# Performance work log

Measured on AMD Instinct MI355X. Metric: run time of the kernel, lower is better.

Reference implementation:

```python
import jax, jax.numpy as jnp
import numpy as np

NUM_USERS = 100000
NUM_ITEMS = 50000
N_NODES = NUM_USERS + NUM_ITEMS
N_EDGES = 2_000_000
D = 64          # embedding_dim
HEADS = 4
F1 = D // HEADS  # per-head out dim of gat1
BATCH = 16384
NEG_SLOPE = 0.2  # PyG GATConv default negative_slope


def setup_inputs() -> dict:
    key = jax.random.key(0)
    ks = jax.random.split(key, 13)
    inp = {}
    inp["edge_index"] = jax.random.randint(ks[0], (2, N_EDGES), 0, N_NODES, dtype=jnp.int64)
    inp["batch_user_idx"] = jax.random.randint(ks[1], (BATCH,), 0, NUM_USERS, dtype=jnp.int64)
    inp["batch_item_idx"] = jax.random.randint(ks[2], (BATCH,), 0, NUM_ITEMS, dtype=jnp.int64)
    # Embedding tables (nn.init.normal_ std=0.01)
    inp["user_emb"] = 0.01 * jax.random.normal(ks[3], (NUM_USERS, D), dtype=jnp.float32)
    inp["item_emb"] = 0.01 * jax.random.normal(ks[4], (NUM_ITEMS, D), dtype=jnp.float32)
    # gat1: GATConv(64, 16, heads=4, concat=True)
    inp["W1"] = jax.random.normal(ks[5], (D, HEADS * F1), dtype=jnp.float32) / np.sqrt(D)
    inp["a_src1"] = jax.random.normal(ks[6], (HEADS, F1), dtype=jnp.float32) / np.sqrt(F1)
    inp["a_dst1"] = jax.random.normal(ks[7], (HEADS, F1), dtype=jnp.float32) / np.sqrt(F1)
    inp["b1"] = jnp.zeros((HEADS * F1,), dtype=jnp.float32)
    # gat2: GATConv(64, 64, heads=1)
    inp["W2"] = jax.random.normal(ks[8], (D, D), dtype=jnp.float32) / np.sqrt(D)
    inp["a_src2"] = jax.random.normal(ks[9], (1, D), dtype=jnp.float32) / np.sqrt(D)
    inp["a_dst2"] = jax.random.normal(ks[10], (1, D), dtype=jnp.float32) / np.sqrt(D)
    inp["b2"] = jnp.zeros((D,), dtype=jnp.float32)
    return inp


def _gat_conv(x, src, dst, W, a_src, a_dst, b, num_nodes):
    """PyG GATConv (eval mode, concat, self-loops already in src/dst)."""
    H, F = a_src.shape
    h = (x @ W).reshape(num_nodes, H, F)                 # [N,H,F]
    alpha_s = jnp.einsum('nhf,hf->nh', h, a_src)         # [N,H]
    alpha_d = jnp.einsum('nhf,hf->nh', h, a_dst)
    e = alpha_s[src] + alpha_d[dst]                      # [E,H]
    e = jax.nn.leaky_relu(e, NEG_SLOPE)
    # scatter-softmax over destination neighborhoods
    m = jax.ops.segment_max(e, dst, num_segments=num_nodes)   # [N,H]
    e = jnp.exp(e - m[dst])
    denom = jax.ops.segment_sum(e, dst, num_segments=num_nodes)
    alpha = e / denom[dst]                               # [E,H]
    msg = h[src] * alpha[:, :, None]                     # [E,H,F]
    agg = jax.ops.segment_sum(msg, dst, num_segments=num_nodes)  # [N,H,F]
    return agg.reshape(num_nodes, H * F) + b


def reference(user_emb, item_emb, W1, a_src1, a_dst1, b1,
              W2, a_src2, a_dst2, b2,
              edge_index, batch_user_idx, batch_item_idx):
    x = jnp.concatenate([user_emb, item_emb], axis=0)    # [N,D]
    n = x.shape[0]
    loop = jnp.arange(n, dtype=edge_index.dtype)          # add_self_loops=True
    src = jnp.concatenate([edge_index[0], loop])
    dst = jnp.concatenate([edge_index[1], loop])
    x = jax.nn.elu(_gat_conv(x, src, dst, W1, a_src1, a_dst1, b1, n))
    x = jax.nn.elu(_gat_conv(x, src, dst, W2, a_src2, a_dst2, b2, n))
    u = x[batch_user_idx]
    v = x[batch_item_idx + NUM_USERS]
    return jax.nn.sigmoid(jnp.sum(u * v, axis=1))        # [BATCH]
```

## Files before the change

kernel.cpp:

```cpp
#include <hip/hip_runtime.h>
#include <math.h>

#define SHIFT 8
#define NBMAX 1024
#define CAP   4096
#define TILE  8192
#define HSCALE 64.0f

typedef float v2f __attribute__((ext_vector_type(2)));
typedef short bf16x8 __attribute__((ext_vector_type(8)));
typedef float f32x4 __attribute__((ext_vector_type(4)));

__device__ __forceinline__ unsigned short f2bf(float f) {
    unsigned u = __float_as_uint(f);
    unsigned r = u + 0x7FFFu + ((u >> 16) & 1u);
    return (unsigned short)(r >> 16);
}
__device__ __forceinline__ unsigned pack2bf(float lo, float hi) {
    return (unsigned)f2bf(lo) | ((unsigned)f2bf(hi) << 16);
}
__device__ __forceinline__ float bflo(unsigned u) { return __uint_as_float(u << 16); }
__device__ __forceinline__ float bfhi(unsigned u) { return __uint_as_float(u & 0xFFFF0000u); }


__global__ __launch_bounds__(512) void k_partition(
    const int* __restrict__ src, const int* __restrict__ dst, int E,
    unsigned* __restrict__ gcur, unsigned* __restrict__ pairs, int NB,
    const float* __restrict__ W1, const float* __restrict__ W2,
    unsigned short* __restrict__ WT1, unsigned short* __restrict__ WT2) {
    __shared__ unsigned lh[NBMAX];
    __shared__ unsigned lcur[NBMAX];
    int t = threadIdx.x;
    {
        int gt = blockIdx.x * 512 + t;
        if (gt < 4096) {
            int n = gt & 63, k = gt >> 6;
            WT1[n * 64 + k] = f2bf(W1[k * 64 + n]);
            WT2[n * 64 + k] = f2bf(W2[k * 64 + n]);
        }
    }
    for (int q = t; q < NB; q += 512) lh[q] = 0;
    __syncthreads();
    int base = blockIdx.x * TILE;
    int end = min(E, base + TILE);
    for (int i = base + t; i < end; i += 512)
        atomicAdd(&lh[((unsigned)dst[i]) >> SHIFT], 1u);
    __syncthreads();
    for (int q = t; q < NB; q += 512) {
        unsigned c = lh[q];
        lcur[q] = c ? ((unsigned)q * CAP + atomicAdd(&gcur[q], c)) : 0u;
    }
    __syncthreads();
    for (int i = base + t; i < end; i += 512) {
        unsigned d = (unsigned)dst[i];
        unsigned pos = atomicAdd(&lcur[d >> SHIFT], 1u);
        pairs[pos] = ((d & 255u) << 18) | (unsigned)src[i];
    }
}

__global__ __launch_bounds__(512) void k_buck_lin(
    const unsigned* __restrict__ pairs, const unsigned* __restrict__ gcur,
    unsigned* __restrict__ beg, unsigned* __restrict__ endd,
    int* __restrict__ srt, int N, int NB,
    const float* __restrict__ xa, const float* __restrict__ xb, int split,
    const unsigned short* __restrict__ WTg,
    const float* __restrict__ a_src, const float* __restrict__ a_dst,
    unsigned char* __restrict__ h, float* __restrict__ as_out,
    float* __restrict__ ad_out) {
    __shared__ union U {
        struct { unsigned lh[256]; unsigned lcur[256]; unsigned sh[256]; int ssrt[CAP]; } b;
        struct { unsigned short sX[64 * 72]; unsigned short sWT[64 * 72]; float sH[64 * 68]; } l;
    } u;
    int t = threadIdx.x;

    if ((int)blockIdx.x < NB) {
        int b = blockIdx.x;
        unsigned s0 = (unsigned)b * CAP;
        int cnt = (int)gcur[b];
        if (t < 256) u.b.lh[t] = 0;
        __syncthreads();
        for (int i = t; i < cnt; i += 512)
            atomicAdd(&u.b.lh[pairs[s0 + i] >> 18], 1u);
        __syncthreads();
        unsigned deg_t = 0;
        if (t < 256) { deg_t = u.b.lh[t]; u.b.sh[t] = deg_t; }
        __syncthreads();
        for (int off = 1; off < 256; off <<= 1) {
            unsigned x = 0;
            if (t < 256 && t >= off) x = u.b.sh[t - off];
            __syncthreads();
            if (t < 256) u.b.sh[t] += x;
            __syncthreads();
        }
        if (t < 256) {
            unsigned excl = u.b.sh[t] - deg_t;
            u.b.lcur[t] = excl;
            int node = (b << SHIFT) + t;
            if (node < N) { beg[node] = s0 + excl; endd[node] = s0 + excl + deg_t; }
        }
        __syncthreads();
        for (int i = t; i < cnt; i += 512) {
            unsigned pk = pairs[s0 + i];
            unsigned p = atomicAdd(&u.b.lcur[pk >> 18], 1u);
            u.b.ssrt[p] = (int)(pk & 0x3FFFFu);
        }
        __syncthreads();
        for (int i = t; i < cnt; i += 512) srt[s0 + i] = u.b.ssrt[i];
    } else {
        int nodeBase = ((int)blockIdx.x - NB) * 64;
        {
            int r = t >> 3, c8 = (t & 7) * 8;
            int n = nodeBase + r;
            float4 v0 = {0,0,0,0}, v1 = {0,0,0,0};
            if (n < N) {
                const float* row = (n < split) ? (xa + (size_t)n * 64 + c8)
                                               : (xb + (size_t)(n - split) * 64 + c8);
                const float4* r4 = (const float4*)row;
                v0 = r4[0]; v1 = r4[1];
            }
            uint4 A = make_uint4(pack2bf(v0.x, v0.y), pack2bf(v0.z, v0.w),
                                 pack2bf(v1.x, v1.y), pack2bf(v1.z, v1.w));
            *(uint4*)(void*)(u.l.sX + r * 72 + c8) = A;
            const uint4* wsrc = (const uint4*)(const void*)WTg;
            *(uint4*)(void*)(u.l.sWT + r * 72 + c8) = wsrc[r * 8 + (c8 >> 3)];
        }
        __syncthreads();
        {
            int lane = t & 63, w = t >> 6;
            if (w < 4) {
                int gl = lane & 15, quad = lane >> 4;
                int m0 = w * 16;
                const bf16x8 a0 = *(const bf16x8*)(void*)(u.l.sX + (m0 + gl) * 72 + quad * 8);
                const bf16x8 a1 = *(const bf16x8*)(void*)(u.l.sX + (m0 + gl) * 72 + 32 + quad * 8);
                f32x4 acc[4];
#pragma unroll
                for (int tt = 0; tt < 4; ++tt) {
                    const bf16x8 b0 = *(const bf16x8*)(void*)(u.l.sWT + (tt * 16 + gl) * 72 + quad * 8);
                    const bf16x8 b1 = *(const bf16x8*)(void*)(u.l.sWT + (tt * 16 + gl) * 72 + 32 + quad * 8);
                    f32x4 c = {0.f, 0.f, 0.f, 0.f};
                    c = __builtin_amdgcn_mfma_f32_16x16x32_bf16(a0, b0, c, 0, 0, 0);
                    c = __builtin_amdgcn_mfma_f32_16x16x32_bf16(a1, b1, c, 0, 0, 0);
                    acc[tt] = c;
                }
#pragma unroll
                for (int tt = 0; tt < 4; ++tt)
#pragma unroll
                    for (int rr = 0; rr < 4; ++rr)
                        u.l.sH[(m0 + quad * 4 + rr) * 68 + tt * 16 + gl] = acc[tt][rr];
            }
        }
        __syncthreads();
        if (t < 256) {
            int m = t >> 2, p = t & 3;
            int n = nodeBase + m;
            const float4* sp = (const float4*)(void*)(u.l.sH + m * 68 + p * 16);
            float4 q0 = sp[0], q1 = sp[1], q2 = sp[2], q3 = sp[3];
            float hv[16] = {q0.x,q0.y,q0.z,q0.w, q1.x,q1.y,q1.z,q1.w,
                            q2.x,q2.y,q2.z,q2.w, q3.x,q3.y,q3.z,q3.w};
            if (n < N) {
                unsigned dwords[4];
#pragma unroll
                for (int q = 0; q < 4; ++q) {
                    int d0 = __builtin_amdgcn_cvt_pk_fp8_f32(hv[4*q] * HSCALE, hv[4*q+1] * HSCALE, 0, false);
                    d0 = __builtin_amdgcn_cvt_pk_fp8_f32(hv[4*q+2] * HSCALE, hv[4*q+3] * HSCALE, d0, true);
                    dwords[q] = (unsigned)d0;
                }
                ((uint4*)h)[(size_t)n * 4 + p] = make_uint4(dwords[0], dwords[1], dwords[2], dwords[3]);
                float ps = 0.f, pd = 0.f;
#pragma unroll
                for (int i = 0; i < 16; ++i) {
                    ps = fmaf(hv[i], a_src[p * 16 + i], ps);
                    pd = fmaf(hv[i], a_dst[p * 16 + i], pd);
                }
                as_out[n * 4 + p] = ps;
                ad_out[n * 4 + p] = pd;
            }
        }
    }
}


template <int HT, int BIN>
__global__ __launch_bounds__(256) void k_linear_mfma(
    const void* __restrict__ xav, const void* __restrict__ xbv, int split,
    const unsigned short* __restrict__ WTg,
    const float* __restrict__ a_src, const float* __restrict__ a_dst,
    unsigned char* __restrict__ h, float* __restrict__ as_out,
    float* __restrict__ ad_out, int N) {
    __shared__ unsigned short sX[64 * 72];
    __shared__ unsigned short sWT[64 * 72];
    __shared__ float sH[64 * 68];
    int t = threadIdx.x;
    int nodeBase = blockIdx.x * 64;

    {
        int r = t >> 2, c4 = (t & 3) * 16;
        int n = nodeBase + r;
        uint4 A = {0,0,0,0}, Bv = {0,0,0,0};
        if (BIN) {
            if (n < N) {
                const unsigned short* row = (const unsigned short*)xav + (size_t)n * 64 + c4;
                A  = ((const uint4*)(const void*)row)[0];
                Bv = ((const uint4*)(const void*)row)[1];
            }
        } else {
            float4 v0 = {0,0,0,0}, v1 = {0,0,0,0}, v2 = {0,0,0,0}, v3 = {0,0,0,0};
            if (n < N) {
                const float* row = (n < split) ? ((const float*)xav + (size_t)n * 64 + c4)
                                               : ((const float*)xbv + (size_t)(n - split) * 64 + c4);
                const float4* r4 = (const float4*)row;
                v0 = r4[0]; v1 = r4[1]; v2 = r4[2]; v3 = r4[3];
            }
            A  = make_uint4(pack2bf(v0.x, v0.y), pack2bf(v0.z, v0.w),
                            pack2bf(v1.x, v1.y), pack2bf(v1.z, v1.w));
            Bv = make_uint4(pack2bf(v2.x, v2.y), pack2bf(v2.z, v2.w),
                            pack2bf(v3.x, v3.y), pack2bf(v3.z, v3.w));
        }
        *(uint4*)(void*)(sX + r * 72 + c4) = A;
        *(uint4*)(void*)(sX + r * 72 + c4 + 8) = Bv;
        const uint4* wsrc = (const uint4*)(const void*)WTg;
        int base = (r * 64 + c4) >> 3;
        *(uint4*)(void*)(sWT + r * 72 + c4) = wsrc[base];
        *(uint4*)(void*)(sWT + r * 72 + c4 + 8) = wsrc[base + 1];
    }
    __syncthreads();

    {
        int lane = t & 63, w = t >> 6;
        int gl = lane & 15, quad = lane >> 4;
        int m0 = w * 16;
        const bf16x8 a0 = *(const bf16x8*)(void*)(sX + (m0 + gl) * 72 + quad * 8);
        const bf16x8 a1 = *(const bf16x8*)(void*)(sX + (m0 + gl) * 72 + 32 + quad * 8);
        f32x4 acc[4];
#pragma unroll
        for (int tt = 0; tt < 4; ++tt) {
            const bf16x8 b0 = *(const bf16x8*)(void*)(sWT + (tt * 16 + gl) * 72 + quad * 8);
            const bf16x8 b1 = *(const bf16x8*)(void*)(sWT + (tt * 16 + gl) * 72 + 32 + quad * 8);
            f32x4 c = {0.f, 0.f, 0.f, 0.f};
            c = __builtin_amdgcn_mfma_f32_16x16x32_bf16(a0, b0, c, 0, 0, 0);
            c = __builtin_amdgcn_mfma_f32_16x16x32_bf16(a1, b1, c, 0, 0, 0);
            acc[tt] = c;
        }
#pragma unroll
        for (int tt = 0; tt < 4; ++tt)
#pragma unroll
            for (int rr = 0; rr < 4; ++rr)
                sH[(m0 + quad * 4 + rr) * 68 + tt * 16 + gl] = acc[tt][rr];
    }
    __syncthreads();

    {
        int m = t >> 2, p = t & 3;
        int n = nodeBase + m;
        const float4* sp = (const float4*)(void*)(sH + m * 68 + p * 16);
        float4 q0 = sp[0], q1 = sp[1], q2 = sp[2], q3 = sp[3];
        float hv[16] = {q0.x,q0.y,q0.z,q0.w, q1.x,q1.y,q1.z,q1.w,
                        q2.x,q2.y,q2.z,q2.w, q3.x,q3.y,q3.z,q3.w};
        if (n < N) {
            unsigned dwords[4];
#pragma unroll
            for (int q = 0; q < 4; ++q) {
                int d0 = __builtin_amdgcn_cvt_pk_fp8_f32(hv[4*q] * HSCALE, hv[4*q+1] * HSCALE, 0, false);
                d0 = __builtin_amdgcn_cvt_pk_fp8_f32(hv[4*q+2] * HSCALE, hv[4*q+3] * HSCALE, d0, true);
                dwords[q] = (unsigned)d0;
            }
            ((uint4*)h)[(size_t)n * 4 + p] = make_uint4(dwords[0], dwords[1], dwords[2], dwords[3]);
            float ps = 0.f, pd = 0.f;
#pragma unroll
            for (int i = 0; i < 16; ++i) {
                ps = fmaf(hv[i], a_src[p * 16 + i], ps);
                pd = fmaf(hv[i], a_dst[p * 16 + i], pd);
            }
            if (HT == 4) {
                as_out[n * 4 + p] = ps;
                ad_out[n * 4 + p] = pd;
            } else {
                ps += __shfl_xor(ps, 1, 64); ps += __shfl_xor(ps, 2, 64);
                pd += __shfl_xor(pd, 1, 64); pd += __shfl_xor(pd, 2, 64);
                if (p == 0) { as_out[n] = ps; ad_out[n] = pd; }
            }
        }
    }
}

template <int HT>
__global__ __launch_bounds__(256, 4) void k_gat(
                      const int* __restrict__ srt, const unsigned* __restrict__ beg,
                      const unsigned* __restrict__ endd,
                      const unsigned* __restrict__ hq, const float* __restrict__ as,
                      const float* __restrict__ ad, const float* __restrict__ b,
                      unsigned* __restrict__ xout, int N) {
    __shared__ unsigned s_vo[4][4][40];
    __shared__ float    s_w[4][4][(HT == 4) ? 164 : 40];

    int t = threadIdx.x;
    int lane = t & 63;
    int wv = t >> 6;
    int gl = lane & 15;
    int g  = lane >> 4;
    int wid = (int)((blockIdx.x * blockDim.x + t) >> 6);
    int d = wid * 4 + g;
    bool active = d < N;
    const int hh = (HT == 4) ? (gl >> 2) : 0;
    const unsigned gl4 = (unsigned)gl << 2;
    const char* hqb = (const char*)hq;
    const char* asb = (const char*)as;

    float adv = 0.f, l = 0.f;
    float a0 = 0.f, a1 = 0.f, a2 = 0.f, a3 = 0.f;
    int kb = 0, end = 0;
    if (active) {
        adv = ad[d * HT + hh];
        float e0 = as[d * HT + hh] + adv;
        e0 = (e0 > 0.f) ? e0 : 0.2f * e0;
        float w0 = __expf(e0);
        unsigned dw = hq[(size_t)d * 16 + gl];
        v2f lo = __builtin_amdgcn_cvt_pk_f32_fp8((int)dw, false);
        v2f hi = __builtin_amdgcn_cvt_pk_f32_fp8((int)dw, true);
        l = w0;
        a0 = w0 * lo.x; a1 = w0 * lo.y; a2 = w0 * hi.x; a3 = w0 * hi.y;
        kb = (int)beg[d];
        end = (int)endd[d];
    }

    int m = end - kb;
    while (__ballot(m > 0)) {
        unsigned v0 = 0, v1 = 0;
        if (gl < m)      v0 = ((unsigned)srt[kb + gl]) << 6;
        if (gl + 16 < m) v1 = ((unsigned)srt[kb + gl + 16]) << 6;

        if (HT == 1) {
            float as0 = 0.f, as1 = 0.f;
            if (gl < m)      as0 = *(const float*)(asb + (v0 >> 4));
            if (gl + 16 < m) as1 = *(const float*)(asb + (v1 >> 4));
            s_vo[wv][g][gl]      = v0;
            s_vo[wv][g][gl + 16] = v1;
            asm volatile("s_waitcnt lgkmcnt(0)" ::: "memory");
            __builtin_amdgcn_sched_barrier(0);
            unsigned rr[32];
            const uint4* vob = (const uint4*)(const void*)&s_vo[wv][g][0];
#pragma unroll
            for (int c = 0; c < 8; ++c) {
                uint4 vv = vob[c];
                rr[4*c+0] = *(const unsigned*)(hqb + (vv.x + gl4));
                rr[4*c+1] = *(const unsigned*)(hqb + (vv.y + gl4));
                rr[4*c+2] = *(const unsigned*)(hqb + (vv.z + gl4));
                rr[4*c+3] = *(const unsigned*)(hqb + (vv.w + gl4));
            }
            float w0 = 0.f, w1 = 0.f;
            if (gl < m) {
                float e = as0 + adv;
                e = (e > 0.f) ? e : 0.2f * e;
                w0 = __expf(e);
            }
            if (gl + 16 < m) {
                float e = as1 + adv;
                e = (e > 0.f) ? e : 0.2f * e;
                w1 = __expf(e);
            }
            float wsum = w0 + w1;
            wsum += __shfl_xor(wsum, 1, 64);
            wsum += __shfl_xor(wsum, 2, 64);
            wsum += __shfl_xor(wsum, 4, 64);
            wsum += __shfl_xor(wsum, 8, 64);
            l += wsum;
            s_w[wv][g][gl]      = w0;
            s_w[wv][g][gl + 16] = w1;
            asm volatile("s_waitcnt lgkmcnt(0)" ::: "memory");
            __builtin_amdgcn_sched_barrier(0);
            const float4* wrd = (const float4*)(const void*)&s_w[wv][g][0];
#pragma unroll
            for (int c = 0; c < 8; ++c) {
                float4 wc = wrd[c];
                float wj[4] = {wc.x, wc.y, wc.z, wc.w};
#pragma unroll
                for (int j = 0; j < 4; ++j) {
                    float w = wj[j];
                    unsigned rv = rr[4*c + j];
                    v2f lo = __builtin_amdgcn_cvt_pk_f32_fp8((int)rv, false);
                    v2f hi = __builtin_amdgcn_cvt_pk_f32_fp8((int)rv, true);
                    a0 = fmaf(w, lo.x, a0);
                    a1 = fmaf(w, lo.y, a1);
                    a2 = fmaf(w, hi.x, a2);
                    a3 = fmaf(w, hi.y, a3);
                }
            }
        } else {
            s_vo[wv][g][gl]      = v0;
            s_vo[wv][g][gl + 16] = v1;
            asm volatile("s_waitcnt lgkmcnt(0)" ::: "memory");
            __builtin_amdgcn_sched_barrier(0);
            int eb = (gl & 3) << 3;
            const uint4* vop = (const uint4*)(const void*)&s_vo[wv][g][eb];
            uint4 va = vop[0], vb = vop[1];
            unsigned vs[8] = {va.x, va.y, va.z, va.w, vb.x, vb.y, vb.z, vb.w};
            float av[8];
#pragma unroll
            for (int r = 0; r < 8; ++r)
                av[r] = *(const float*)(asb + ((vs[r] >> 2) + ((unsigned)hh << 2)));
            unsigned rr[32];
            const uint4* vob = (const uint4*)(const void*)&s_vo[wv][g][0];
#pragma unroll
            for (int c = 0; c < 8; ++c) {
                uint4 vv = vob[c];
                rr[4*c+0] = *(const unsigned*)(hqb + (vv.x + gl4));
                rr[4*c+1] = *(const unsigned*)(hqb + (vv.y + gl4));
                rr[4*c+2] = *(const unsigned*)(hqb + (vv.z + gl4));
                rr[4*c+3] = *(const unsigned*)(hqb + (vv.w + gl4));
            }
            float wq[8];
#pragma unroll
            for (int r = 0; r < 8; ++r) {
                wq[r] = 0.f;
                if (eb + r < m) {
                    float e = av[r] + adv;
                    e = (e > 0.f) ? e : 0.2f * e;
                    wq[r] = __expf(e);
                }
            }
            float wsum = ((wq[0] + wq[1]) + (wq[2] + wq[3]))
                       + ((wq[4] + wq[5]) + (wq[6] + wq[7]));
            wsum += __shfl_xor(wsum, 1, 64);
            wsum += __shfl_xor(wsum, 2, 64);
            l += wsum;
            float4* wp = (float4*)(void*)&s_w[wv][g][hh * 40 + eb];
            wp[0] = make_float4(wq[0], wq[1], wq[2], wq[3]);
            wp[1] = make_float4(wq[4], wq[5], wq[6], wq[7]);
            asm volatile("s_waitcnt lgkmcnt(0)" ::: "memory");
            __builtin_amdgcn_sched_barrier(0);
            const float4* wrd = (const float4*)(const void*)&s_w[wv][g][hh * 40];
#pragma unroll
            for (int c = 0; c < 8; ++c) {
                float4 wc = wrd[c];
                float wj[4] = {wc.x, wc.y, wc.z, wc.w};
#pragma unroll
                for (int j = 0; j < 4; ++j) {
                    float w = wj[j];
                    unsigned rv = rr[4*c + j];
                    v2f lo = __builtin_amdgcn_cvt_pk_f32_fp8((int)rv, false);
                    v2f hi = __builtin_amdgcn_cvt_pk_f32_fp8((int)rv, true);
                    a0 = fmaf(w, lo.x, a0);
                    a1 = fmaf(w, lo.y, a1);
                    a2 = fmaf(w, hi.x, a2);
                    a3 = fmaf(w, hi.y, a3);
                }
            }
        }
        kb += 32;
        m = end - kb;
    }

    if (active) {
        float4 bb4 = ((const float4*)b)[gl];
        float rs = 1.f / (l * HSCALE);
        float v0 = a0 * rs + bb4.x;
        float v1 = a1 * rs + bb4.y;
        float v2 = a2 * rs + bb4.z;
        float v3 = a3 * rs + bb4.w;
        float o0 = (v0 > 0.f) ? v0 : expm1f(v0);
        float o1 = (v1 > 0.f) ? v1 : expm1f(v1);
        float o2 = (v2 > 0.f) ? v2 : expm1f(v2);
        float o3 = (v3 > 0.f) ? v3 : expm1f(v3);
        ((uint2*)xout)[(size_t)d * 16 + gl] = make_uint2(pack2bf(o0, o1), pack2bf(o2, o3));
    }
}

__global__ void k_dot_sig(const uint2* __restrict__ x2, const int* __restrict__ uidx,
                          const int* __restrict__ vidx, float* __restrict__ out,
                          int batch, int numUsers) {
    int lane = threadIdx.x & 63;
    int gl = lane & 15;
    int q = (int)(((blockIdx.x * blockDim.x + threadIdx.x) >> 6) * 4 + (lane >> 4));
    if (q >= batch) return;
    int u = uidx[q];
    int v = vidx[q] + numUsers;
    uint2 a = x2[(size_t)u * 16 + gl];
    uint2 c = x2[(size_t)v * 16 + gl];
    float p = bflo(a.x) * bflo(c.x) + bfhi(a.x) * bfhi(c.x)
            + bflo(a.y) * bflo(c.y) + bfhi(a.y) * bfhi(c.y);
#pragma unroll
    for (int off = 1; off < 16; off <<= 1) p += __shfl_xor(p, off, 64);
    if (gl == 0) out[q] = 1.f / (1.f + __expf(-p));
}


static inline int cdiv(long long a, long long b) { return (int)((a + b - 1) / b); }

extern "C" void kernel_launch(void* const* d_in, const int* in_sizes, int n_in,
                              void* d_out, int out_size, void* d_ws, size_t ws_size,
                              hipStream_t stream) {
    const int* edge_index = (const int*)d_in[0];
    const int* buidx      = (const int*)d_in[1];
    const int* biidx      = (const int*)d_in[2];
    const float* user_emb = (const float*)d_in[3];
    const float* item_emb = (const float*)d_in[4];
    const float* W1     = (const float*)d_in[5];
    const float* a_src1 = (const float*)d_in[6];
    const float* a_dst1 = (const float*)d_in[7];
    const float* b1     = (const float*)d_in[8];
    const float* W2     = (const float*)d_in[9];
    const float* a_src2 = (const float*)d_in[10];
    const float* a_dst2 = (const float*)d_in[11];
    const float* b2     = (const float*)d_in[12];
    float* out = (float*)d_out;

    const int E  = in_sizes[0] / 2;
    const int B  = in_sizes[1];
    const int NU = in_sizes[3] / 64;
    const int NI = in_sizes[4] / 64;
    const int N  = NU + NI;
    const int NB = cdiv(N, 1 << SHIFT);

    const int* src = edge_index;
    const int* dst = edge_index + E;

    float* ws = (float*)d_ws;
    size_t off = 0;
    unsigned* x_buf  = (unsigned*)(ws + off); off += (size_t)N * 32;
    unsigned* h_buf  = (unsigned*)(ws + off); off += (size_t)N * 16;
    float*    as_b   = ws + off; off += (size_t)N * 4;
    float*    ad_b   = ws + off; off += (size_t)N * 4;
    unsigned* gcur_b = (unsigned*)(ws + off); off += NBMAX;
    unsigned* beg_b  = (unsigned*)(ws + off); off += (size_t)N;
    unsigned* end_b  = (unsigned*)(ws + off); off += (size_t)N;
    unsigned* pairs_b= (unsigned*)(ws + off); off += (size_t)NB * CAP;
    int*      srt_b  = (int*)(ws + off); off += (size_t)NB * CAP;
    unsigned short* wt1_b = (unsigned short*)(ws + off); off += 2048;
    unsigned short* wt2_b = (unsigned short*)(ws + off); off += 2048;

    const int BS = 256;

    hipMemsetAsync(gcur_b, 0, NBMAX * sizeof(unsigned), stream);
    k_partition<<<cdiv(E, TILE), 512, 0, stream>>>(src, dst, E, gcur_b, pairs_b, NB,
                                                   W1, W2, wt1_b, wt2_b);

    k_buck_lin<<<NB + cdiv(N, 64), 512, 0, stream>>>(
        pairs_b, gcur_b, beg_b, end_b, srt_b, N, NB,
        user_emb, item_emb, NU, wt1_b, a_src1, a_dst1,
        (unsigned char*)h_buf, as_b, ad_b);

    k_gat<4><<<cdiv((long long)N * 16, BS), BS, 0, stream>>>(
        srt_b, beg_b, end_b, h_buf, as_b, ad_b, b1, x_buf, N);

    k_linear_mfma<1, 1><<<cdiv(N, 64), BS, 0, stream>>>(x_buf, x_buf, N, wt2_b,
                                                        a_src2, a_dst2,
                                                        (unsigned char*)h_buf, as_b, ad_b, N);
    k_gat<1><<<cdiv((long long)N * 16, BS), BS, 0, stream>>>(
        srt_b, beg_b, end_b, h_buf, as_b, ad_b, b2, x_buf, N);

    k_dot_sig<<<cdiv((long long)B * 16, BS), BS, 0, stream>>>(
        (const uint2*)x_buf, buidx, biidx, out, B, NU);
}
```

Baseline: 248.8 us.

## Stage partitioned edge pairs in LDS before coalesced bucket writes

The partition kernel now runs a block-local prefix scan over bucket counts and scatters each edge into a shared-memory staging buffer ordered by bucket. It then writes the staged pairs to global memory sequentially, so consecutive threads store to contiguous addresses within each bucket instead of scattering randomly. This adds a 1024-entry scan with many barriers and about 48KB of extra LDS per block, which may reduce occupancy. It also assumes NB is at most 1024, because the per-bucket arrays are indexed directly by thread.

After: 240.7 us (median of 2 runs). 1.03x faster.

```diff
diff --git a/kernel.cpp b/kernel.cpp
--- a/kernel.cpp
+++ b/kernel.cpp
@@ -29,7 +29,10 @@
     const float* __restrict__ W1, const float* __restrict__ W2,
     unsigned short* __restrict__ WT1, unsigned short* __restrict__ WT2) {
     __shared__ unsigned lh[NBMAX];
-    __shared__ unsigned lcur[NBMAX];
+    __shared__ unsigned lbase[NBMAX];
+    __shared__ unsigned gbase[NBMAX];
+    __shared__ unsigned spair[TILE];
+    __shared__ unsigned short sb[TILE];
     int t = threadIdx.x;
     {
         int gt = blockIdx.x * 512 + t;
@@ -39,22 +42,45 @@
             WT2[n * 64 + k] = f2bf(W2[k * 64 + n]);
         }
     }
-    for (int q = t; q < NB; q += 512) lh[q] = 0;
+    lh[t] = 0; lh[t + 512] = 0;
     __syncthreads();
     int base = blockIdx.x * TILE;
     int end = min(E, base + TILE);
     for (int i = base + t; i < end; i += 512)
         atomicAdd(&lh[((unsigned)dst[i]) >> SHIFT], 1u);
     __syncthreads();
-    for (int q = t; q < NB; q += 512) {
-        unsigned c = lh[q];
-        lcur[q] = c ? ((unsigned)q * CAP + atomicAdd(&gcur[q], c)) : 0u;
+    lbase[t] = lh[t]; lbase[t + 512] = lh[t + 512];
+    __syncthreads();
+    for (int off = 1; off < 1024; off <<= 1) {
+        unsigned a0 = (t >= off) ? lbase[t - off] : 0u;
+        unsigned a1 = ((t + 512) >= off) ? lbase[t + 512 - off] : 0u;
+        __syncthreads();
+        lbase[t] += a0;
+        lbase[t + 512] += a1;
+        __syncthreads();
+    }
+    {
+        unsigned c0 = lh[t], c1 = lh[t + 512];
+        unsigned e0 = lbase[t] - c0, e1 = lbase[t + 512] - c1;
+        if (c0) gbase[t] = (unsigned)t * CAP + atomicAdd(&gcur[t], c0);
+        if (c1) gbase[t + 512] = (unsigned)(t + 512) * CAP + atomicAdd(&gcur[t + 512], c1);
+        __syncthreads();
+        lbase[t] = e0; lbase[t + 512] = e1;
+        lh[t] = e0; lh[t + 512] = e1;
     }
     __syncthreads();
     for (int i = base + t; i < end; i += 512) {
         unsigned d = (unsigned)dst[i];
-        unsigned pos = atomicAdd(&lcur[d >> SHIFT], 1u);
-        pairs[pos] = ((d & 255u) << 18) | (unsigned)src[i];
+        unsigned b = d >> SHIFT;
+        unsigned p = atomicAdd(&lh[b], 1u);
+        spair[p] = ((d & 255u) << 18) | (unsigned)src[i];
+        sb[p] = (unsigned short)b;
+    }
+    __syncthreads();
+    int cnt = end - base;
+    for (int i = t; i < cnt; i += 512) {
+        unsigned b = sb[i];
+        pairs[gbase[b] + ((unsigned)i - lbase[b])] = spair[i];
     }
 }
 
```
